# Kernel optimization log

Measured on AMD Instinct MI355X. Metric: run time of the kernel, lower is better.

The kernel has to match this reference:

```python
import jax, jax.numpy as jnp
import numpy as np

O, I, B, H, W = 128, 128, 32, 112, 112
STRIDE, PAD = 1, 1

def _synth_weight(core, periphery, threshold, scale):
    # core: (O,I,1,1); periphery: (8,); threshold: (O,); scale: (1,)
    c = core[:, :, 0, 0]                                   # (O,I) center tap
    # threshold-gated scale: soft gate on periphery contribution per (o,i)
    gate = jax.nn.sigmoid(scale[0] * (jnp.abs(c) - threshold[:, None]))  # (O,I)
    # 9 flattened taps: index 4 is center (weight 1), others use shared periphery
    p_full = jnp.concatenate([periphery[:4], jnp.ones((1,), c.dtype), periphery[4:]])  # (9,)
    is_center = (jnp.arange(9) == 4).astype(c.dtype)        # (9,)
    gate_k = is_center[None, None, :] + (1.0 - is_center)[None, None, :] * gate[:, :, None]
    w = c[:, :, None] * p_full[None, None, :] * gate_k      # (O,I,9)
    return w.reshape(c.shape[0], c.shape[1], 3, 3)          # (O,I,3,3)

def setup_inputs() -> dict:
    key = jax.random.key(0)
    kx, kc, kp = jax.random.split(key, 3)
    x = jax.random.normal(kx, (B, I, H, W), dtype=jnp.float32)
    # kaiming-uniform-ish core init
    bound = float(np.sqrt(6.0 / I))
    core = jax.random.uniform(kc, (O, I, 1, 1), minval=-bound, maxval=bound, dtype=jnp.float32)
    periphery = jax.random.uniform(kp, (8,), minval=-0.1, maxval=0.1, dtype=jnp.float32)
    threshold = jnp.full((O,), 0.1, dtype=jnp.float32)
    scale = jnp.array([10.0], dtype=jnp.float32)
    return {"x": x, "core": core, "periphery": periphery, "threshold": threshold, "scale": scale}

def reference(x, core, periphery, threshold, scale):
    w = _synth_weight(core, periphery, threshold, scale)    # (O,I,3,3)
    return jax.lax.conv_general_dilated(
        x, w,
        window_strides=(STRIDE, STRIDE),
        padding=[(PAD, PAD), (PAD, PAD)],
        dimension_numbers=("NCHW", "OIHW", "NCHW"),
    )
```

## Files before the change

### kernel.cpp

```cpp
#include <hip/hip_runtime.h>

typedef short short8 __attribute__((ext_vector_type(8)));
typedef float f32x4 __attribute__((ext_vector_type(4)));
typedef unsigned short ushort8_t __attribute__((ext_vector_type(8)));

#define O_CH 128
#define I_CH 128
#define HW 112
#define PLANE (HW * HW)
#define NCOL 114
#define BUFB (3 * NCOL * 64)

__device__ __forceinline__ unsigned short f2bf(float f) {
  union { float f; unsigned u; } v; v.f = f;
  unsigned r = v.u + 0x7FFFu + ((v.u >> 16) & 1u);
  return (unsigned short)(r >> 16);
}

__device__ __forceinline__ unsigned pktrunc(float lo, float hi) {
  union { float f; unsigned u; } a, b; a.f = lo; b.f = hi;
  return __builtin_amdgcn_perm(b.u, a.u, 0x07060302u);
}

__global__ void wsynth_kernel(const float* __restrict__ core,
                              const float* __restrict__ periph,
                              const float* __restrict__ thr,
                              const float* __restrict__ scale,
                              unsigned short* __restrict__ Wb) {
  int idx = blockIdx.x * blockDim.x + threadIdx.x;
  if (idx >= O_CH * I_CH) return;
  int o = idx >> 7;
  float c = core[idx];
  float s = scale[0];
  float g = 1.0f / (1.0f + __expf(-s * (fabsf(c) - thr[o])));
#pragma unroll
  for (int tap = 0; tap < 9; ++tap) {
    float p  = (tap == 4) ? 1.0f : periph[tap < 4 ? tap : tap - 1];
    float gg = (tap == 4) ? 1.0f : g;
    Wb[tap * (O_CH * I_CH) + idx] = f2bf(c * p * gg);
  }
}

__global__ __launch_bounds__(256, 3)
void conv_kernel(const float* __restrict__ X,
                 const unsigned short* __restrict__ Wb,
                 float* __restrict__ Out) {
  __shared__ unsigned short Xs[2 * 3 * NCOL * 32];
  char* lds = (char*)Xs;

  const int bid = blockIdx.x;
  const int L = (bid & 7) * 448 + (bid >> 3);
  const int b = L / HW;
  const int y = L - b * HW;

  const int t   = threadIdx.x;
  const int wv  = t >> 6;
  const int l   = t & 63;
  const int ln  = l & 15;
  const int lk4 = l >> 4;

  const int c    = t & 127;
  const int chb  = (t >> 7) * 16;
  const int icol = c - 1;
  const bool cok = (c < NCOL);
  const int wxor = (c & 3) ^ (((c >> 2) & 1) << 1);

  f32x4 acc[2][7];
#pragma unroll
  for (int mr = 0; mr < 2; ++mr)
#pragma unroll
    for (int nf = 0; nf < 7; ++nf)
      acc[mr][nf] = (f32x4)0.0f;

#define LOAD16(V, KCH, SUB)                                                     \
  {                                                                             \
    const int row_ = y + (SUB)-1;                                               \
    const bool ok_ = (row_ >= 0) && (row_ < HW) && (icol >= 0) && (icol < HW);  \
    const float* sp_ = X + ((size_t)(b * I_CH + (KCH) + chb) * HW + row_) * HW  \
                       + icol;                                                  \
    _Pragma("unroll") for (int j = 0; j < 16; ++j) V[j] = 0.0f;                 \
    if (ok_) {                                                                  \
      _Pragma("unroll") for (int j = 0; j < 16; ++j) V[j] = sp_[j * PLANE];     \
    }                                                                           \
  }

#define WRITE16(V, SUB, WB)                                                     \
  if (cok) {                                                                    \
    const int base_ = ((SUB)*NCOL + c) * 64;                                    \
    _Pragma("unroll") for (int q = 0; q < 2; ++q) {                             \
      union { ushort8_t s; unsigned u[4]; } pk_;                                \
      pk_.u[0] = pktrunc(V[q * 8 + 0], V[q * 8 + 1]);                           \
      pk_.u[1] = pktrunc(V[q * 8 + 2], V[q * 8 + 3]);                           \
      pk_.u[2] = pktrunc(V[q * 8 + 4], V[q * 8 + 5]);                           \
      pk_.u[3] = pktrunc(V[q * 8 + 6], V[q * 8 + 7]);                           \
      const int slot_ = ((chb >> 3) + q) ^ wxor;                                \
      *reinterpret_cast<ushort8_t*>((WB) + base_ + slot_ * 16) = pk_.s;         \
    }                                                                           \
  }

#define COMPUTE_SUB(SUB, RB, K)                                                 \
  _Pragma("unroll") for (int dx = 0; dx < 3; ++dx) {                            \
    const int tap_ = (SUB)*3 + dx;                                              \
    const unsigned short* wp_ = Wb + tap_ * (O_CH * I_CH)                       \
                              + (wv * 32 + ln) * I_CH + (K)*32 + lk4 * 8;       \
    short8 a0_ = *reinterpret_cast<const short8*>(wp_);                         \
    short8 a1_ = *reinterpret_cast<const short8*>(wp_ + 16 * I_CH);             \
    const int cc_ = dx + ln;                                                    \
    const int rslot_ = lk4 ^ (cc_ & 3) ^ (((cc_ >> 2) & 1) << 1);               \
    const char* bp_ = (RB) + ((SUB)*NCOL + cc_) * 64 + rslot_ * 16;             \
    _Pragma("unroll") for (int nf = 0; nf < 7; ++nf) {                          \
      short8 bb_ = *reinterpret_cast<const short8*>(bp_ + nf * 1024);           \
      acc[0][nf] = __builtin_amdgcn_mfma_f32_16x16x32_bf16(a0_, bb_, acc[0][nf], 0, 0, 0); \
      acc[1][nf] = __builtin_amdgcn_mfma_f32_16x16x32_bf16(a1_, bb_, acc[1][nf], 0, 0, 0); \
    }                                                                           \
  }

  {
    float P0[16], P1[16], P2[16];
    LOAD16(P0, 0, 0)
    LOAD16(P1, 0, 1)
    LOAD16(P2, 0, 2)
    WRITE16(P0, 0, lds)
    WRITE16(P1, 1, lds)
    WRITE16(P2, 2, lds)
  }
  __syncthreads();

#pragma unroll
  for (int k = 0; k < 4; ++k) {
    char* rbuf = lds + (k & 1) * BUFB;
    char* wbuf = lds + ((k & 1) ^ 1) * BUFB;
    float LA[16], LB[16];

    if (k < 3) LOAD16(LA, (k + 1) * 32, 0)
    COMPUTE_SUB(0, rbuf, k)

    if (k < 3) LOAD16(LB, (k + 1) * 32, 1)
    COMPUTE_SUB(1, rbuf, k)
    if (k < 3) WRITE16(LA, 0, wbuf)

    if (k < 3) LOAD16(LA, (k + 1) * 32, 2)
    COMPUTE_SUB(2, rbuf, k)
    if (k < 3) {
      WRITE16(LB, 1, wbuf)
      WRITE16(LA, 2, wbuf)
      __syncthreads();
    }
  }

  const int obase = wv * 32 + lk4 * 4;
  float* outp = Out + (size_t)b * O_CH * PLANE + (size_t)y * HW;
#pragma unroll
  for (int mr = 0; mr < 2; ++mr) {
#pragma unroll
    for (int j = 0; j < 4; ++j) {
      const int o = obase + mr * 16 + j;
      float* po = outp + (size_t)o * PLANE;
#pragma unroll
      for (int nf = 0; nf < 7; ++nf) {
        po[nf * 16 + ln] = acc[mr][nf][j];
      }
    }
  }
}

extern "C" void kernel_launch(void* const* d_in, const int* in_sizes, int n_in,
                              void* d_out, int out_size, void* d_ws, size_t ws_size,
                              hipStream_t stream) {
  const float* x      = (const float*)d_in[0];
  const float* core   = (const float*)d_in[1];
  const float* periph = (const float*)d_in[2];
  const float* thr    = (const float*)d_in[3];
  const float* scale  = (const float*)d_in[4];
  unsigned short* Wb  = (unsigned short*)d_ws;

  wsynth_kernel<<<(O_CH * I_CH + 255) / 256, 256, 0, stream>>>(core, periph, thr, scale, Wb);

  const int grid = 32 * HW;
  conv_kernel<<<grid, 256, 0, stream>>>(x, Wb, (float*)d_out);
}
```

Baseline: 207.0 us.

## Split each output row into two 56-column tiles to raise occupancy

Each block now computes half an output row (56 columns padded to 64) instead of a full 112-column row, doubling the grid. Accumulators and LDS staging shrink, and launch bounds rise to 4 blocks per SM to improve latency hiding. In exchange, about an eighth of MFMA work is spent on padded columns and halo input columns are loaded twice.

```diff
diff --git a/kernel.cpp b/kernel.cpp
--- a/kernel.cpp
+++ b/kernel.cpp
@@ -8,8 +8,9 @@
 #define I_CH 128
 #define HW 112
 #define PLANE (HW * HW)
-#define NCOL 114
-#define BUFB (3 * NCOL * 64)
+#define COLS 56
+#define NSTG 66
+#define BUFB (3 * NSTG * 64)
 
 __device__ __forceinline__ unsigned short f2bf(float f) {
   union { float f; unsigned u; } v; v.f = f;
@@ -41,17 +42,19 @@
   }
 }
 
-__global__ __launch_bounds__(256, 3)
+__global__ __launch_bounds__(256, 4)
 void conv_kernel(const float* __restrict__ X,
                  const unsigned short* __restrict__ Wb,
                  float* __restrict__ Out) {
-  __shared__ unsigned short Xs[2 * 3 * NCOL * 32];
+  __shared__ unsigned short Xs[2 * 3 * NSTG * 32];
   char* lds = (char*)Xs;
 
   const int bid = blockIdx.x;
-  const int L = (bid & 7) * 448 + (bid >> 3);
-  const int b = L / HW;
-  const int y = L - b * HW;
+  const int L = (bid & 7) * 896 + (bid >> 3);
+  const int b = L / 224;
+  const int rem = L - b * 224;
+  const int y = rem >> 1;
+  const int cb = (rem & 1) * COLS;
 
   const int t   = threadIdx.x;
   const int wv  = t >> 6;
@@ -59,43 +62,39 @@
   const int ln  = l & 15;
   const int lk4 = l >> 4;
 
-  const int c    = t & 127;
-  const int chb  = (t >> 7) * 16;
-  const int icol = c - 1;
-  const bool cok = (c < NCOL);
-  const int wxor = (c & 3) ^ (((c >> 2) & 1) << 1);
+  const int s    = t & 63;
+  const int grp  = t >> 6;
+  const int icol = cb - 1 + s;
+  const bool sok = (s < 58);
+  const int wslot = grp ^ ((s >> 1) & 3);
 
-  f32x4 acc[2][7];
+  f32x4 acc[2][4];
 #pragma unroll
   for (int mr = 0; mr < 2; ++mr)
 #pragma unroll
-    for (int nf = 0; nf < 7; ++nf)
+    for (int nf = 0; nf < 4; ++nf)
       acc[mr][nf] = (f32x4)0.0f;
 
-#define LOAD16(V, KCH, SUB)                                                     \
+#define LOAD8(V, KCH, SUB)                                                      \
   {                                                                             \
     const int row_ = y + (SUB)-1;                                               \
     const bool ok_ = (row_ >= 0) && (row_ < HW) && (icol >= 0) && (icol < HW);  \
-    const float* sp_ = X + ((size_t)(b * I_CH + (KCH) + chb) * HW + row_) * HW  \
-                       + icol;                                                  \
-    _Pragma("unroll") for (int j = 0; j < 16; ++j) V[j] = 0.0f;                 \
+    const float* sp_ = X + ((size_t)(b * I_CH + (KCH) + grp * 8) * HW + row_)   \
+                       * HW + icol;                                             \
+    _Pragma("unroll") for (int j = 0; j < 8; ++j) V[j] = 0.0f;                  \
     if (ok_) {                                                                  \
-      _Pragma("unroll") for (int j = 0; j < 16; ++j) V[j] = sp_[j * PLANE];     \
+      _Pragma("unroll") for (int j = 0; j < 8; ++j) V[j] = sp_[j * PLANE];      \
     }                                                                           \
   }
 
-#define WRITE16(V, SUB, WB)                                                     \
-  if (cok) {                                                                    \
-    const int base_ = ((SUB)*NCOL + c) * 64;                                    \
-    _Pragma("unroll") for (int q = 0; q < 2; ++q) {                             \
-      union { ushort8_t s; unsigned u[4]; } pk_;                                \
-      pk_.u[0] = pktrunc(V[q * 8 + 0], V[q * 8 + 1]);                           \
-      pk_.u[1] = pktrunc(V[q * 8 + 2], V[q * 8 + 3]);                           \
-      pk_.u[2] = pktrunc(V[q * 8 + 4], V[q * 8 + 5]);                           \
-      pk_.u[3] = pktrunc(V[q * 8 + 6], V[q * 8 + 7]);                           \
-      const int slot_ = ((chb >> 3) + q) ^ wxor;                                \
-      *reinterpret_cast<ushort8_t*>((WB) + base_ + slot_ * 16) = pk_.s;         \
-    }                                                                           \
+#define WRITE8(V, SUB, WB)                                                      \
+  if (sok) {                                                                    \
+    union { ushort8_t v8; unsigned u[4]; } pk_;                                 \
+    pk_.u[0] = pktrunc(V[0], V[1]);                                             \
+    pk_.u[1] = pktrunc(V[2], V[3]);                                             \
+    pk_.u[2] = pktrunc(V[4], V[5]);                                             \
+    pk_.u[3] = pktrunc(V[6], V[7]);                                             \
+    *reinterpret_cast<ushort8_t*>((WB) + ((SUB)*NSTG + s) * 64 + wslot * 16) = pk_.v8; \
   }
 
 #define COMPUTE_SUB(SUB, RB, K)                                                 \
@@ -105,24 +104,24 @@
                               + (wv * 32 + ln) * I_CH + (K)*32 + lk4 * 8;       \
     short8 a0_ = *reinterpret_cast<const short8*>(wp_);                         \
     short8 a1_ = *reinterpret_cast<const short8*>(wp_ + 16 * I_CH);             \
-    const int cc_ = dx + ln;                                                    \
-    const int rslot_ = lk4 ^ (cc_ & 3) ^ (((cc_ >> 2) & 1) << 1);               \
-    const char* bp_ = (RB) + ((SUB)*NCOL + cc_) * 64 + rslot_ * 16;             \
-    _Pragma("unroll") for (int nf = 0; nf < 7; ++nf) {                          \
-      short8 bb_ = *reinterpret_cast<const short8*>(bp_ + nf * 1024);           \
+    const int q_ = dx + ln;                                                     \
+    const int rslot_ = lk4 ^ ((q_ >> 1) & 3);    \
+    const char* bp_ = (RB) + ((SUB)*NSTG + q_) * 64 + rslot_ * 16;              \
+    _Pragma("unroll") for (int nf = 0; nf < 4; ++nf) {                          \
+      short8 bb_ = *reinterpret_cast<const short8*>(bp_ + nf * (16 * 64));      \
       acc[0][nf] = __builtin_amdgcn_mfma_f32_16x16x32_bf16(a0_, bb_, acc[0][nf], 0, 0, 0); \
       acc[1][nf] = __builtin_amdgcn_mfma_f32_16x16x32_bf16(a1_, bb_, acc[1][nf], 0, 0, 0); \
     }                                                                           \
   }
 
   {
-    float P0[16], P1[16], P2[16];
-    LOAD16(P0, 0, 0)
-    LOAD16(P1, 0, 1)
-    LOAD16(P2, 0, 2)
-    WRITE16(P0, 0, lds)
-    WRITE16(P1, 1, lds)
-    WRITE16(P2, 2, lds)
+    float P0[8], P1[8], P2[8];
+    LOAD8(P0, 0, 0)
+    LOAD8(P1, 0, 1)
+    LOAD8(P2, 0, 2)
+    WRITE8(P0, 0, lds)
+    WRITE8(P1, 1, lds)
+    WRITE8(P2, 2, lds)
   }
   __syncthreads();
 
@@ -130,26 +129,26 @@
   for (int k = 0; k < 4; ++k) {
     char* rbuf = lds + (k & 1) * BUFB;
     char* wbuf = lds + ((k & 1) ^ 1) * BUFB;
-    float LA[16], LB[16];
+    float LA[8], LB[8];
 
-    if (k < 3) LOAD16(LA, (k + 1) * 32, 0)
+    if (k < 3) LOAD8(LA, (k + 1) * 32, 0)
     COMPUTE_SUB(0, rbuf, k)
 
-    if (k < 3) LOAD16(LB, (k + 1) * 32, 1)
+    if (k < 3) LOAD8(LB, (k + 1) * 32, 1)
     COMPUTE_SUB(1, rbuf, k)
-    if (k < 3) WRITE16(LA, 0, wbuf)
+    if (k < 3) WRITE8(LA, 0, wbuf)
 
-    if (k < 3) LOAD16(LA, (k + 1) * 32, 2)
+    if (k < 3) LOAD8(LA, (k + 1) * 32, 2)
     COMPUTE_SUB(2, rbuf, k)
     if (k < 3) {
-      WRITE16(LB, 1, wbuf)
-      WRITE16(LA, 2, wbuf)
+      WRITE8(LB, 1, wbuf)
+      WRITE8(LA, 2, wbuf)
       __syncthreads();
     }
   }
 
   const int obase = wv * 32 + lk4 * 4;
-  float* outp = Out + (size_t)b * O_CH * PLANE + (size_t)y * HW;
+  float* outp = Out + (size_t)b * O_CH * PLANE + (size_t)y * HW + cb;
 #pragma unroll
   for (int mr = 0; mr < 2; ++mr) {
 #pragma unroll
@@ -157,8 +156,10 @@
       const int o = obase + mr * 16 + j;
       float* po = outp + (size_t)o * PLANE;
 #pragma unroll
-      for (int nf = 0; nf < 7; ++nf) {
-        po[nf * 16 + ln] = acc[mr][nf][j];
+      for (int nf = 0; nf < 4; ++nf) {
+        if (nf < 3 || ln < 8) {
+          po[nf * 16 + ln] = acc[mr][nf][j];
+        }
       }
     }
   }
@@ -176,6 +177,6 @@
 
   wsynth_kernel<<<(O_CH * I_CH + 255) / 256, 256, 0, stream>>>(core, periph, thr, scale, Wb);
 
-  const int grid = 32 * HW;
+  const int grid = 32 * HW * 2;
   conv_kernel<<<grid, 256, 0, stream>>>(x, Wb, (float*)d_out);
 }
```

Measured after the change: 315.9 us. 52.6% more time.

## Replace double-buffered LDS with 4-slot ring pipeline and raise occupancy

Applied to the files above, without the earlier changes.

Restructures the conv input staging from two 3-row buffers into a 4-slot ring of single row-chunks, cycled over 12 phases. Each phase prefetches the chunk two phases ahead into registers and writes the next chunk into LDS before a barrier. The LDS footprint shrinks, so launch bounds rise from 3 to 4 blocks per SIMD, and s_setprio is added around the MFMA sections. The intent is better latency hiding and occupancy, at the cost of 11 barriers instead of 3, a new swizzle pattern, and register pressure under the tighter launch bound.

```diff
diff --git a/kernel.cpp b/kernel.cpp
--- a/kernel.cpp
+++ b/kernel.cpp
@@ -9,7 +9,7 @@
 #define HW 112
 #define PLANE (HW * HW)
 #define NCOL 114
-#define BUFB (3 * NCOL * 64)
+#define SLOTB (NCOL * 64)
 
 __device__ __forceinline__ unsigned short f2bf(float f) {
   union { float f; unsigned u; } v; v.f = f;
@@ -41,11 +41,11 @@
   }
 }
 
-__global__ __launch_bounds__(256, 3)
+__global__ __launch_bounds__(256, 4)
 void conv_kernel(const float* __restrict__ X,
                  const unsigned short* __restrict__ Wb,
                  float* __restrict__ Out) {
-  __shared__ unsigned short Xs[2 * 3 * NCOL * 32];
+  __shared__ unsigned short Xs[4 * NCOL * 32];
   char* lds = (char*)Xs;
 
   const int bid = blockIdx.x;
@@ -59,11 +59,11 @@
   const int ln  = l & 15;
   const int lk4 = l >> 4;
 
-  const int c    = t & 127;
-  const int chb  = (t >> 7) * 16;
-  const int icol = c - 1;
-  const bool cok = (c < NCOL);
-  const int wxor = (c & 3) ^ (((c >> 2) & 1) << 1);
+  const int col  = t & 127;
+  const int half = t >> 7;
+  const int icol = col - 1;
+  const bool cok = (col < NCOL);
+  const int wsw  = (col >> 1) & 3;
 
   f32x4 acc[2][7];
 #pragma unroll
@@ -72,80 +72,84 @@
     for (int nf = 0; nf < 7; ++nf)
       acc[mr][nf] = (f32x4)0.0f;
 
-#define LOAD16(V, KCH, SUB)                                                     \
+#define LOAD16(V, TP)                                                           \
   {                                                                             \
-    const int row_ = y + (SUB)-1;                                               \
+    const int row_ = y + ((TP) % 3) - 1;                                        \
     const bool ok_ = (row_ >= 0) && (row_ < HW) && (icol >= 0) && (icol < HW);  \
-    const float* sp_ = X + ((size_t)(b * I_CH + (KCH) + chb) * HW + row_) * HW  \
-                       + icol;                                                  \
+    const float* sp_ = X + ((size_t)(b * I_CH + ((TP) / 3) * 32 + half * 16)    \
+                            * HW + row_) * HW + icol;                           \
     _Pragma("unroll") for (int j = 0; j < 16; ++j) V[j] = 0.0f;                 \
     if (ok_) {                                                                  \
       _Pragma("unroll") for (int j = 0; j < 16; ++j) V[j] = sp_[j * PLANE];     \
     }                                                                           \
   }
 
-#define WRITE16(V, SUB, WB)                                                     \
+#define WRITE16(V, TP)                                                          \
   if (cok) {                                                                    \
-    const int base_ = ((SUB)*NCOL + c) * 64;                                    \
+    char* base_ = lds + ((TP) & 3) * SLOTB + col * 64;                          \
     _Pragma("unroll") for (int q = 0; q < 2; ++q) {                             \
       union { ushort8_t s; unsigned u[4]; } pk_;                                \
       pk_.u[0] = pktrunc(V[q * 8 + 0], V[q * 8 + 1]);                           \
       pk_.u[1] = pktrunc(V[q * 8 + 2], V[q * 8 + 3]);                           \
       pk_.u[2] = pktrunc(V[q * 8 + 4], V[q * 8 + 5]);                           \
       pk_.u[3] = pktrunc(V[q * 8 + 6], V[q * 8 + 7]);                           \
-      const int slot_ = ((chb >> 3) + q) ^ wxor;                                \
-      *reinterpret_cast<ushort8_t*>((WB) + base_ + slot_ * 16) = pk_.s;         \
+      const int slot_ = (half * 2 + q) ^ wsw;                                   \
+      *reinterpret_cast<ushort8_t*>(base_ + slot_ * 16) = pk_.s;                \
     }                                                                           \
   }
 
-#define COMPUTE_SUB(SUB, RB, K)                                                 \
-  _Pragma("unroll") for (int dx = 0; dx < 3; ++dx) {                            \
-    const int tap_ = (SUB)*3 + dx;                                              \
-    const unsigned short* wp_ = Wb + tap_ * (O_CH * I_CH)                       \
-                              + (wv * 32 + ln) * I_CH + (K)*32 + lk4 * 8;       \
-    short8 a0_ = *reinterpret_cast<const short8*>(wp_);                         \
-    short8 a1_ = *reinterpret_cast<const short8*>(wp_ + 16 * I_CH);             \
-    const int cc_ = dx + ln;                                                    \
-    const int rslot_ = lk4 ^ (cc_ & 3) ^ (((cc_ >> 2) & 1) << 1);               \
-    const char* bp_ = (RB) + ((SUB)*NCOL + cc_) * 64 + rslot_ * 16;             \
-    _Pragma("unroll") for (int nf = 0; nf < 7; ++nf) {                          \
-      short8 bb_ = *reinterpret_cast<const short8*>(bp_ + nf * 1024);           \
-      acc[0][nf] = __builtin_amdgcn_mfma_f32_16x16x32_bf16(a0_, bb_, acc[0][nf], 0, 0, 0); \
-      acc[1][nf] = __builtin_amdgcn_mfma_f32_16x16x32_bf16(a1_, bb_, acc[1][nf], 0, 0, 0); \
+#define COMPUTE_PHASE(P)                                                        \
+  {                                                                             \
+    const char* sb_ = lds + ((P) & 3) * SLOTB;                                  \
+    __builtin_amdgcn_s_setprio(1);                                              \
+    _Pragma("unroll") for (int dx = 0; dx < 3; ++dx) {                          \
+      const int tap_ = ((P) % 3) * 3 + dx;                                      \
+      const unsigned short* wp_ = Wb + tap_ * (O_CH * I_CH)                     \
+                                + (wv * 32 + ln) * I_CH + ((P) / 3) * 32        \
+                                + lk4 * 8;                                      \
+      short8 a0_ = *reinterpret_cast<const short8*>(wp_);                       \
+      short8 a1_ = *reinterpret_cast<const short8*>(wp_ + 16 * I_CH);           \
+      const int q_ = dx + ln;                                                   \
+      const int rslot_ = lk4 ^ ((q_ >> 1) & 3);    \
+      const char* bp_ = sb_ + q_ * 64 + rslot_ * 16;                            \
+      _Pragma("unroll") for (int nf = 0; nf < 7; ++nf) {                        \
+        short8 bb_ = *reinterpret_cast<const short8*>(bp_ + nf * 1024);         \
+        acc[0][nf] = __builtin_amdgcn_mfma_f32_16x16x32_bf16(a0_, bb_, acc[0][nf], 0, 0, 0); \
+        acc[1][nf] = __builtin_amdgcn_mfma_f32_16x16x32_bf16(a1_, bb_, acc[1][nf], 0, 0, 0); \
+      }                                                                         \
     }                                                                           \
+    __builtin_amdgcn_s_setprio(0);                                              \
   }
 
+#define RING_BARRIER()                                                          \
+  {                                                                             \
+    asm volatile("s_waitcnt lgkmcnt(0)" ::: "memory");                          \
+    __builtin_amdgcn_s_barrier();                                               \
+    __builtin_amdgcn_sched_barrier(0);                                          \
+  }
+
+  float LD[16];
+
   {
-    float P0[16], P1[16], P2[16];
-    LOAD16(P0, 0, 0)
-    LOAD16(P1, 0, 1)
-    LOAD16(P2, 0, 2)
-    WRITE16(P0, 0, lds)
-    WRITE16(P1, 1, lds)
-    WRITE16(P2, 2, lds)
+    float P0[16];
+    LOAD16(P0, 0) WRITE16(P0, 0)
+    LOAD16(P0, 1) WRITE16(P0, 1)
+    LOAD16(P0, 2) WRITE16(P0, 2)
   }
-  __syncthreads();
+  LOAD16(LD, 3)
+  RING_BARRIER()
 
 #pragma unroll
-  for (int k = 0; k < 4; ++k) {
-    char* rbuf = lds + (k & 1) * BUFB;
-    char* wbuf = lds + ((k & 1) ^ 1) * BUFB;
-    float LA[16], LB[16];
-
-    if (k < 3) LOAD16(LA, (k + 1) * 32, 0)
-    COMPUTE_SUB(0, rbuf, k)
-
-    if (k < 3) LOAD16(LB, (k + 1) * 32, 1)
-    COMPUTE_SUB(1, rbuf, k)
-    if (k < 3) WRITE16(LA, 0, wbuf)
-
-    if (k < 3) LOAD16(LA, (k + 1) * 32, 2)
-    COMPUTE_SUB(2, rbuf, k)
-    if (k < 3) {
-      WRITE16(LB, 1, wbuf)
-      WRITE16(LA, 2, wbuf)
-      __syncthreads();
+  for (int p = 0; p < 12; ++p) {
+    float NL[16];
+    if (p <= 7) LOAD16(NL, p + 4)
+    COMPUTE_PHASE(p)
+    if (p <= 8) WRITE16(LD, p + 3)
+    if (p <= 7) {
+#pragma unroll
+      for (int j = 0; j < 16; ++j) LD[j] = NL[j];
     }
+    if (p <= 10) RING_BARRIER()
   }
 
   const int obase = wv * 32 + lk4 * 4;
```

New measurement: 272.3 us. 31.5% more time.

## Retile conv waves to 64x64 output blocks with simpler LDS swizzle

Applied to the files above, without the earlier changes.

Changes the per-wave MFMA tiling from 32 output channels by 112 columns to a 2x2 wave grid covering 64 channels by 64 (or 48) columns. This raises A-fragment reuse and cuts B-fragment LDS reads per MFMA, and replaces the LDS XOR swizzle with a simpler (c>>1)&3 pattern. In exchange the waves become unbalanced (the second column group does 3 of 4 fragments), and the extra weight loads raise register pressure.

```diff
diff --git a/kernel.cpp b/kernel.cpp
--- a/kernel.cpp
+++ b/kernel.cpp
@@ -58,19 +58,24 @@
   const int l   = t & 63;
   const int ln  = l & 15;
   const int lk4 = l >> 4;
+  const int mi  = wv >> 1;
+  const int ng  = wv & 1;
+  const int cb  = ng * 64;
 
   const int c    = t & 127;
   const int chb  = (t >> 7) * 16;
   const int icol = c - 1;
   const bool cok = (c < NCOL);
-  const int wxor = (c & 3) ^ (((c >> 2) & 1) << 1);
-
-  f32x4 acc[2][7];
-#pragma unroll
-  for (int mr = 0; mr < 2; ++mr)
-#pragma unroll
-    for (int nf = 0; nf < 7; ++nf)
-      acc[mr][nf] = (f32x4)0.0f;
+  const int wxor = (c >> 1) & 3;
+
+  f32x4 acc[4][4];
+#pragma unroll
+  for (int mt = 0; mt < 4; ++mt)
+#pragma unroll
+    for (int nf = 0; nf < 4; ++nf)
+      acc[mt][nf] = (f32x4)0.0f;
+
+  const unsigned short* wbase = Wb + (mi * 64 + ln) * I_CH + lk4 * 8;
 
 #define LOAD16(V, KCH, SUB)                                                     \
   {                                                                             \
@@ -98,20 +103,38 @@
     }                                                                           \
   }
 
-#define COMPUTE_SUB(SUB, RB, K)                                                 \
+#define COMPUTE_SUB2(SUB, RB, K)                                                \
   _Pragma("unroll") for (int dx = 0; dx < 3; ++dx) {                            \
-    const int tap_ = (SUB)*3 + dx;                                              \
-    const unsigned short* wp_ = Wb + tap_ * (O_CH * I_CH)                       \
-                              + (wv * 32 + ln) * I_CH + (K)*32 + lk4 * 8;       \
-    short8 a0_ = *reinterpret_cast<const short8*>(wp_);                         \
-    short8 a1_ = *reinterpret_cast<const short8*>(wp_ + 16 * I_CH);             \
-    const int cc_ = dx + ln;                                                    \
-    const int rslot_ = lk4 ^ (cc_ & 3) ^ (((cc_ >> 2) & 1) << 1);               \
-    const char* bp_ = (RB) + ((SUB)*NCOL + cc_) * 64 + rslot_ * 16;             \
-    _Pragma("unroll") for (int nf = 0; nf < 7; ++nf) {                          \
-      short8 bb_ = *reinterpret_cast<const short8*>(bp_ + nf * 1024);           \
-      acc[0][nf] = __builtin_amdgcn_mfma_f32_16x16x32_bf16(a0_, bb_, acc[0][nf], 0, 0, 0); \
-      acc[1][nf] = __builtin_amdgcn_mfma_f32_16x16x32_bf16(a1_, bb_, acc[1][nf], 0, 0, 0); \
+    const unsigned short* wp_ = wbase + ((SUB)*3 + dx) * (O_CH * I_CH)          \
+                              + (K)*32;                                         \
+    short8 A0_ = *reinterpret_cast<const short8*>(wp_);                         \
+    short8 A1_ = *reinterpret_cast<const short8*>(wp_ + 16 * I_CH);             \
+    short8 A2_ = *reinterpret_cast<const short8*>(wp_ + 32 * I_CH);             \
+    short8 A3_ = *reinterpret_cast<const short8*>(wp_ + 48 * I_CH);             \
+    const int q_ = cb + dx + ln;                                                \
+    const int rslot_ = lk4 ^ ((q_ >> 1) & 3);     \
+    const char* bp_ = (RB) + ((SUB)*NCOL + q_) * 64 + rslot_ * 16;              \
+    short8 b0_ = *reinterpret_cast<const short8*>(bp_);                         \
+    short8 b1_ = *reinterpret_cast<const short8*>(bp_ + 1024);                  \
+    short8 b2_ = *reinterpret_cast<const short8*>(bp_ + 2048);                  \
+    acc[0][0] = __builtin_amdgcn_mfma_f32_16x16x32_bf16(A0_, b0_, acc[0][0], 0, 0, 0); \
+    acc[1][0] = __builtin_amdgcn_mfma_f32_16x16x32_bf16(A1_, b0_, acc[1][0], 0, 0, 0); \
+    acc[2][0] = __builtin_amdgcn_mfma_f32_16x16x32_bf16(A2_, b0_, acc[2][0], 0, 0, 0); \
+    acc[3][0] = __builtin_amdgcn_mfma_f32_16x16x32_bf16(A3_, b0_, acc[3][0], 0, 0, 0); \
+    acc[0][1] = __builtin_amdgcn_mfma_f32_16x16x32_bf16(A0_, b1_, acc[0][1], 0, 0, 0); \
+    acc[1][1] = __builtin_amdgcn_mfma_f32_16x16x32_bf16(A1_, b1_, acc[1][1], 0, 0, 0); \
+    acc[2][1] = __builtin_amdgcn_mfma_f32_16x16x32_bf16(A2_, b1_, acc[2][1], 0, 0, 0); \
+    acc[3][1] = __builtin_amdgcn_mfma_f32_16x16x32_bf16(A3_, b1_, acc[3][1], 0, 0, 0); \
+    acc[0][2] = __builtin_amdgcn_mfma_f32_16x16x32_bf16(A0_, b2_, acc[0][2], 0, 0, 0); \
+    acc[1][2] = __builtin_amdgcn_mfma_f32_16x16x32_bf16(A1_, b2_, acc[1][2], 0, 0, 0); \
+    acc[2][2] = __builtin_amdgcn_mfma_f32_16x16x32_bf16(A2_, b2_, acc[2][2], 0, 0, 0); \
+    acc[3][2] = __builtin_amdgcn_mfma_f32_16x16x32_bf16(A3_, b2_, acc[3][2], 0, 0, 0); \
+    if (ng == 0) {                                                              \
+      short8 b3_ = *reinterpret_cast<const short8*>(bp_ + 3072);                \
+      acc[0][3] = __builtin_amdgcn_mfma_f32_16x16x32_bf16(A0_, b3_, acc[0][3], 0, 0, 0); \
+      acc[1][3] = __builtin_amdgcn_mfma_f32_16x16x32_bf16(A1_, b3_, acc[1][3], 0, 0, 0); \
+      acc[2][3] = __builtin_amdgcn_mfma_f32_16x16x32_bf16(A2_, b3_, acc[2][3], 0, 0, 0); \
+      acc[3][3] = __builtin_amdgcn_mfma_f32_16x16x32_bf16(A3_, b3_, acc[3][3], 0, 0, 0); \
     }                                                                           \
   }
 
@@ -133,14 +156,14 @@
     float LA[16], LB[16];
 
     if (k < 3) LOAD16(LA, (k + 1) * 32, 0)
-    COMPUTE_SUB(0, rbuf, k)
+    COMPUTE_SUB2(0, rbuf, k)
 
     if (k < 3) LOAD16(LB, (k + 1) * 32, 1)
-    COMPUTE_SUB(1, rbuf, k)
+    COMPUTE_SUB2(1, rbuf, k)
     if (k < 3) WRITE16(LA, 0, wbuf)
 
     if (k < 3) LOAD16(LA, (k + 1) * 32, 2)
-    COMPUTE_SUB(2, rbuf, k)
+    COMPUTE_SUB2(2, rbuf, k)
     if (k < 3) {
       WRITE16(LB, 1, wbuf)
       WRITE16(LA, 2, wbuf)
@@ -148,17 +171,18 @@
     }
   }
 
-  const int obase = wv * 32 + lk4 * 4;
-  float* outp = Out + (size_t)b * O_CH * PLANE + (size_t)y * HW;
-#pragma unroll
-  for (int mr = 0; mr < 2; ++mr) {
+  float* outp = Out + (size_t)b * O_CH * PLANE + (size_t)y * HW + cb;
+#pragma unroll
+  for (int mt = 0; mt < 4; ++mt) {
 #pragma unroll
     for (int j = 0; j < 4; ++j) {
-      const int o = obase + mr * 16 + j;
+      const int o = mi * 64 + mt * 16 + lk4 * 4 + j;
       float* po = outp + (size_t)o * PLANE;
 #pragma unroll
-      for (int nf = 0; nf < 7; ++nf) {
-        po[nf * 16 + ln] = acc[mr][nf][j];
+      for (int nf = 0; nf < 4; ++nf) {
+        if (nf < 3 || ng == 0) {
+          po[nf * 16 + ln] = acc[mt][nf][j];
+        }
       }
     }
   }
```

Result: slower. 313.1 us (+51.2%).
